# Performance work log

Measured on AMD Instinct MI355X. Metric: run time of the kernel, lower is better.

## Reference

```python
import jax, jax.numpy as jnp
import numpy as np

EPS = 1e-8
N_ITERS = 3
LN_EPS = 1e-5  # torch LayerNorm default


def layer_norm(x, g, b):
    mu = jnp.mean(x, axis=-1, keepdims=True)
    var = jnp.var(x, axis=-1, keepdims=True)
    return (x - mu) / jnp.sqrt(var + LN_EPS) * g + b


def setup_inputs() -> dict:
    key = jax.random.key(0)
    ks = jax.random.split(key, 12)
    B, S, F, D_in, D_slot, D_kvq, D_hid = 64, 16, 4096, 512, 512, 512, 2048
    p = lambda i, shape: jax.random.normal(ks[i], shape, dtype=jnp.float32) * 0.02
    return dict(
        slots=jax.random.normal(ks[0], (B, S, D_slot), dtype=jnp.float32),
        features=jax.random.normal(ks[1], (B, F, D_in), dtype=jnp.float32),
        ln_feat_g=jnp.ones((D_in,), jnp.float32), ln_feat_b=jnp.zeros((D_in,), jnp.float32),
        ln_slot_g=jnp.ones((D_slot,), jnp.float32), ln_slot_b=jnp.zeros((D_slot,), jnp.float32),
        w_k=p(2, (D_kvq, D_in)), w_v=p(3, (D_kvq, D_in)), w_q=p(4, (D_kvq, D_slot)),
        gru_w_ih=p(5, (3 * D_slot, D_kvq)), gru_w_hh=p(6, (3 * D_slot, D_slot)),
        gru_b_ih=jnp.zeros((3 * D_slot,), jnp.float32), gru_b_hh=jnp.zeros((3 * D_slot,), jnp.float32),
        mlp_ln_g=jnp.ones((D_slot,), jnp.float32), mlp_ln_b=jnp.zeros((D_slot,), jnp.float32),
        mlp_w1=p(7, (D_hid, D_slot)), mlp_b1=jnp.zeros((D_hid,), jnp.float32),
        mlp_w2=p(8, (D_slot, D_hid)), mlp_b2=jnp.zeros((D_slot,), jnp.float32),
    )


def reference(slots, features, ln_feat_g, ln_feat_b, ln_slot_g, ln_slot_b,
              w_k, w_v, w_q, gru_w_ih, gru_w_hh, gru_b_ih, gru_b_hh,
              mlp_ln_g, mlp_ln_b, mlp_w1, mlp_b1, mlp_w2, mlp_b2):
    scale = w_q.shape[0] ** -0.5  # kvq_dim**-0.5

    f = layer_norm(features, ln_feat_g, ln_feat_b)  # [B,F,D_in]
    keys = f @ w_k.T    # [B,F,D_kvq]
    values = f @ w_v.T  # [B,F,D_kvq]

    def gru_cell(x, h):  # torch.nn.GRUCell semantics
        gi = x @ gru_w_ih.T + gru_b_ih
        gh = h @ gru_w_hh.T + gru_b_hh
        i_r, i_z, i_n = jnp.split(gi, 3, axis=-1)
        h_r, h_z, h_n = jnp.split(gh, 3, axis=-1)
        r = jax.nn.sigmoid(i_r + h_r)
        z = jax.nn.sigmoid(i_z + h_z)
        n = jnp.tanh(i_n + r * h_n)
        return (1.0 - z) * n + z * h

    pre_norm_attn = None
    for _ in range(N_ITERS):  # fixed small iteration count (n_iters=3)
        s_n = layer_norm(slots, ln_slot_g, ln_slot_b)  # note: GRU hidden uses normed slots, per source
        q = s_n @ w_q.T                                 # [B,S,D_kvq]
        dots = jnp.einsum('bsd,bfd->bsf', q, keys) * scale
        pre_norm_attn = jax.nn.softmax(dots, axis=1)    # softmax over SLOT dim
        attn = pre_norm_attn + EPS
        attn = attn / jnp.sum(attn, axis=-1, keepdims=True)
        updates = jnp.einsum('bsf,bfd->bsd', attn, values)
        slots = gru_cell(updates, s_n)
        # residual MLP with initial LayerNorm
        h = layer_norm(slots, mlp_ln_g, mlp_ln_b)
        h = jax.nn.relu(h @ mlp_w1.T + mlp_b1) @ mlp_w2.T + mlp_b2
        slots = slots + h
    return slots, pre_norm_attn
```

## Files before the change

kernel.cpp:

```cpp
#include <hip/hip_runtime.h>


typedef __bf16 bf16x8 __attribute__((ext_vector_type(8)));
typedef float  f32x4  __attribute__((ext_vector_type(4)));

#define DEV static __device__ __forceinline__

DEV float bf2f_lo(unsigned int u) { union { unsigned int i; float f; } v; v.i = u << 16; return v.f; }
DEV unsigned short f2bf(float f) {
  union { float f; unsigned int i; } v; v.f = f;
  return (unsigned short)((v.i + 0x7FFFu + ((v.i >> 16) & 1u)) >> 16);
}

template<int OUTF>
__global__ __launch_bounds__(256) void ln512_kernel(
    const float* __restrict__ X, const float* __restrict__ g,
    const float* __restrict__ b, unsigned short* __restrict__ Yb,
    float* __restrict__ Yf, int R) {
  int wave = (blockIdx.x << 2) | (threadIdx.x >> 6);
  int lane = threadIdx.x & 63;
  if (wave >= R) return;
  const float4* xp = reinterpret_cast<const float4*>(X + (size_t)wave * 512);
  float4 x0 = xp[lane * 2], x1 = xp[lane * 2 + 1];
  float xv[8] = {x0.x, x0.y, x0.z, x0.w, x1.x, x1.y, x1.z, x1.w};
  float s = 0.f, q = 0.f;
#pragma unroll
  for (int j = 0; j < 8; ++j) { s += xv[j]; q += xv[j] * xv[j]; }
#pragma unroll
  for (int off = 32; off; off >>= 1) { s += __shfl_xor(s, off); q += __shfl_xor(q, off); }
  float mu = s * (1.0f / 512.0f);
  float var = q * (1.0f / 512.0f) - mu * mu;
  float rstd = rsqrtf(var + 1e-5f);
  const float4* gp = reinterpret_cast<const float4*>(g);
  const float4* bp = reinterpret_cast<const float4*>(b);
  float4 g0 = gp[lane * 2], g1 = gp[lane * 2 + 1];
  float4 b0 = bp[lane * 2], b1 = bp[lane * 2 + 1];
  float gv[8] = {g0.x, g0.y, g0.z, g0.w, g1.x, g1.y, g1.z, g1.w};
  float bv[8] = {b0.x, b0.y, b0.z, b0.w, b1.x, b1.y, b1.z, b1.w};
  float y[8];
  unsigned short u[8];
#pragma unroll
  for (int j = 0; j < 8; ++j) { y[j] = (xv[j] - mu) * rstd * gv[j] + bv[j]; u[j] = f2bf(y[j]); }
  uint4 o = make_uint4(
      (unsigned)u[0] | ((unsigned)u[1] << 16), (unsigned)u[2] | ((unsigned)u[3] << 16),
      (unsigned)u[4] | ((unsigned)u[5] << 16), (unsigned)u[6] | ((unsigned)u[7] << 16));
  reinterpret_cast<uint4*>(Yb + (size_t)wave * 512)[lane] = o;
  if (OUTF) {
    float4* yf = reinterpret_cast<float4*>(Yf + (size_t)wave * 512);
    yf[lane * 2]     = make_float4(y[0], y[1], y[2], y[3]);
    yf[lane * 2 + 1] = make_float4(y[4], y[5], y[6], y[7]);
  }
}

__global__ __launch_bounds__(256) void prep_weights_kernel(
    const float* __restrict__ w_ih, const float* __restrict__ w_hh,
    const float* __restrict__ w1, const float* __restrict__ w2,
    const float* __restrict__ w_k, const float* __restrict__ w_q,
    const float* __restrict__ w_v,
    unsigned short* __restrict__ Wih, unsigned short* __restrict__ Whh,
    unsigned short* __restrict__ W1, unsigned short* __restrict__ W2,
    unsigned short* __restrict__ WkT, unsigned short* __restrict__ WqT,
    unsigned short* __restrict__ WvT) {
  int blk = blockIdx.x, tid = threadIdx.x;
  if (blk < 3584) {
    const float* src; unsigned short* dst; int base;
    if (blk < 768)       { src = w_ih; dst = Wih; base = blk; }
    else if (blk < 1536) { src = w_hh; dst = Whh; base = blk - 768; }
    else if (blk < 2560) { src = w1;   dst = W1;  base = blk - 1536; }
    else                 { src = w2;   dst = W2;  base = blk - 2560; }
    int i = base * 256 + tid;
    float4 v = reinterpret_cast<const float4*>(src)[i];
    unsigned int lo = (unsigned)f2bf(v.x) | ((unsigned)f2bf(v.y) << 16);
    unsigned int hi = (unsigned)f2bf(v.z) | ((unsigned)f2bf(v.w) << 16);
    reinterpret_cast<uint2*>(dst)[i] = make_uint2(lo, hi);
  } else {
    int rgn = (blk - 3584) >> 10, base = (blk - 3584) & 1023;
    const float* src = rgn == 0 ? w_k : rgn == 1 ? w_q : w_v;
    unsigned short* dst = rgn == 0 ? WkT : rgn == 1 ? WqT : WvT;
    int t2 = base * 256 + tid;
    int i = t2 >> 9, j = t2 & 511;
    dst[t2] = f2bf(src[j * 512 + i]);
  }
}

template<int MODE>
__global__ __launch_bounds__(256) void gemm_nt(
    const unsigned short* __restrict__ A, const unsigned short* __restrict__ Bm,
    const float* __restrict__ bias, unsigned short* __restrict__ Cb,
    int M, int N, int K) {
  int lane = threadIdx.x & 63;
  int w = threadIdx.x >> 6;
  int m0 = blockIdx.y << 5;
  int n0 = (blockIdx.x << 7) + (w << 5);
  int lo = lane & 15, hi = lane >> 4;
  const unsigned short* Ap = A + (size_t)(m0 + lo) * K + (hi << 3);
  const unsigned short* Bp = Bm + (size_t)(n0 + lo) * K + (hi << 3);
  f32x4 acc[2][2];
#pragma unroll
  for (int i = 0; i < 2; ++i)
#pragma unroll
    for (int j = 0; j < 2; ++j) acc[i][j] = f32x4{0.f, 0.f, 0.f, 0.f};
#pragma unroll 2
  for (int kk = 0; kk < K; kk += 32) {
    bf16x8 a0 = *reinterpret_cast<const bf16x8*>(Ap + kk);
    bf16x8 a1 = *reinterpret_cast<const bf16x8*>(Ap + (size_t)16 * K + kk);
    bf16x8 b0 = *reinterpret_cast<const bf16x8*>(Bp + kk);
    bf16x8 b1 = *reinterpret_cast<const bf16x8*>(Bp + (size_t)16 * K + kk);
    acc[0][0] = __builtin_amdgcn_mfma_f32_16x16x32_bf16(a0, b0, acc[0][0], 0, 0, 0);
    acc[0][1] = __builtin_amdgcn_mfma_f32_16x16x32_bf16(a0, b1, acc[0][1], 0, 0, 0);
    acc[1][0] = __builtin_amdgcn_mfma_f32_16x16x32_bf16(a1, b0, acc[1][0], 0, 0, 0);
    acc[1][1] = __builtin_amdgcn_mfma_f32_16x16x32_bf16(a1, b1, acc[1][1], 0, 0, 0);
  }
#pragma unroll
  for (int i = 0; i < 2; ++i)
#pragma unroll
    for (int j = 0; j < 2; ++j) {
      int col = n0 + (j << 4) + lo;
      float bvv = (MODE == 3) ? bias[col] : 0.f;
#pragma unroll
      for (int r = 0; r < 4; ++r) {
        int row = m0 + (i << 4) + (hi << 2) + r;
        float v = acc[i][j][r];
        if (MODE == 0) Cb[(size_t)row * N + col] = f2bf(v);
        else           Cb[(size_t)row * N + col] = f2bf(fmaxf(v + bvv, 0.f));
      }
    }
}

template<int MODE>
__global__ __launch_bounds__(256) void gemm_nt64(
    const unsigned short* __restrict__ A, const unsigned short* __restrict__ Bm,
    const float* __restrict__ bias, const float* __restrict__ res,
    float* __restrict__ Cf, unsigned short* __restrict__ Cb,
    int M, int N, int K) {
  int lane = threadIdx.x & 63;
  int w = threadIdx.x >> 6;
  int m0 = (blockIdx.y << 5) + ((w >> 1) << 4);
  int n0 = (blockIdx.x << 6) + ((w & 1) << 5);
  int lo = lane & 15, hi = lane >> 4;
  const unsigned short* Ap = A + (size_t)(m0 + lo) * K + (hi << 3);
  const unsigned short* Bp = Bm + (size_t)(n0 + lo) * K + (hi << 3);
  f32x4 acc[2];
  acc[0] = f32x4{0.f, 0.f, 0.f, 0.f};
  acc[1] = f32x4{0.f, 0.f, 0.f, 0.f};
#pragma unroll 2
  for (int kk = 0; kk < K; kk += 32) {
    bf16x8 a0 = *reinterpret_cast<const bf16x8*>(Ap + kk);
    bf16x8 b0 = *reinterpret_cast<const bf16x8*>(Bp + kk);
    bf16x8 b1 = *reinterpret_cast<const bf16x8*>(Bp + (size_t)16 * K + kk);
    acc[0] = __builtin_amdgcn_mfma_f32_16x16x32_bf16(a0, b0, acc[0], 0, 0, 0);
    acc[1] = __builtin_amdgcn_mfma_f32_16x16x32_bf16(a0, b1, acc[1], 0, 0, 0);
  }
#pragma unroll
  for (int j = 0; j < 2; ++j) {
    int col = n0 + (j << 4) + lo;
    float bvv = (MODE == 4) ? bias[col] : 0.f;
#pragma unroll
    for (int r = 0; r < 4; ++r) {
      int row = m0 + (hi << 2) + r;
      float v = acc[j][r];
      if (MODE == 0) Cb[(size_t)row * N + col] = f2bf(v);
      else Cf[(size_t)row * N + col] = v + bvv + res[(size_t)row * N + col];
    }
  }
}

__global__ __launch_bounds__(128) void fused_attn_kernel(
    const unsigned short* __restrict__ Qp,
    const unsigned short* __restrict__ Fn,
    float* __restrict__ Upart,
    float* __restrict__ fsumP,
    float* __restrict__ attn_out) {
  __shared__ unsigned short tile[32 * 514];
  __shared__ unsigned short attn_lds[16 * 34];
  int b = blockIdx.y, g = blockIdx.x;
  int t = threadIdx.x;
  int w = t >> 6, lane = t & 63;
  int lo = lane & 15, hi = lane >> 4;
  unsigned int* tile32 = reinterpret_cast<unsigned int*>(tile);

  const unsigned short* qa = Qp + ((size_t)b * 16 + lo) * 512 + (hi << 3);
  const unsigned short* gstage = Fn + ((size_t)b * 4096 + g * 256) * 512;

  f32x4 uacc[16];
#pragma unroll
  for (int s = 0; s < 16; ++s) uacc[s] = f32x4{0.f, 0.f, 0.f, 0.f};
  float fs[4] = {0.f, 0.f, 0.f, 0.f};

  const float scale = 0.04419417382415922f;

  {
    uint4 nx[16];
#pragma unroll
    for (int k = 0; k < 16; ++k)
      nx[k] = *reinterpret_cast<const uint4*>(gstage + (size_t)t * 8 + k * 1024);
#pragma unroll
    for (int k = 0; k < 16; ++k) {
      unsigned int* p32 = tile32 + (k * 2 + w) * 257 + lane * 4;
      p32[0] = nx[k].x; p32[1] = nx[k].y; p32[2] = nx[k].z; p32[3] = nx[k].w;
    }
  }
  __syncthreads();

  for (int c = 0; c < 8; ++c) {
    uint4 nx[16];
    if (c < 7) {
      const unsigned short* src = gstage + (size_t)(c + 1) * 16384;
#pragma unroll
      for (int k = 0; k < 16; ++k)
        nx[k] = *reinterpret_cast<const uint4*>(src + (size_t)t * 8 + k * 1024);
    }
    f32x4 dacc = {0.f, 0.f, 0.f, 0.f};
#pragma unroll
    for (int ks = 0; ks < 16; ++ks) {
      const unsigned int* bp32 = tile32 + (w * 16 + lo) * 257 + ks * 16 + (hi << 2);
      union { unsigned int u[4]; bf16x8 v; } bf;
      bf.u[0] = bp32[0]; bf.u[1] = bp32[1]; bf.u[2] = bp32[2]; bf.u[3] = bp32[3];
      bf16x8 a = *reinterpret_cast<const bf16x8*>(qa + ks * 32);
      dacc = __builtin_amdgcn_mfma_f32_16x16x32_bf16(a, bf.v, dacc, 0, 0, 0);
    }
    float d4[4], mx = -3.4e38f;
#pragma unroll
    for (int r = 0; r < 4; ++r) { d4[r] = dacc[r] * scale; mx = fmaxf(mx, d4[r]); }
    mx = fmaxf(mx, __shfl_xor(mx, 16));
    mx = fmaxf(mx, __shfl_xor(mx, 32));
    float e4[4], ss = 0.f;
#pragma unroll
    for (int r = 0; r < 4; ++r) { e4[r] = __expf(d4[r] - mx); ss += e4[r]; }
    ss += __shfl_xor(ss, 16);
    ss += __shfl_xor(ss, 32);
    float inv = 1.f / ss;
    float cs[4];
#pragma unroll
    for (int r = 0; r < 4; ++r) {
      float p = e4[r] * inv;
      if (attn_out)
        attn_out[((size_t)b * 16 + (hi << 2) + r) * 4096 + g * 256 + c * 32 + (w << 4) + lo] = p;
      unsigned short uu = f2bf(p + 1e-8f);
      attn_lds[((hi << 2) + r) * 34 + (w << 4) + lo] = uu;
      cs[r] = bf2f_lo(uu);
    }
#pragma unroll
    for (int m = 1; m < 16; m <<= 1) {
#pragma unroll
      for (int r = 0; r < 4; ++r) cs[r] += __shfl_xor(cs[r], m);
    }
#pragma unroll
    for (int r = 0; r < 4; ++r) fs[r] += cs[r];
    __syncthreads();
    {
      const unsigned int* ap32 = reinterpret_cast<const unsigned int*>(attn_lds) + lo * 17 + (hi << 2);
      union { unsigned int u[4]; bf16x8 v; } paf;
      paf.u[0] = ap32[0]; paf.u[1] = ap32[1]; paf.u[2] = ap32[2]; paf.u[3] = ap32[3];
#pragma unroll
      for (int sub = 0; sub < 16; ++sub) {
        int dcol = (w << 8) + (sub << 4) + lo;
        union { unsigned short u[8]; bf16x8 v; } pbf;
#pragma unroll
        for (int j = 0; j < 8; ++j)
          pbf.u[j] = tile[((hi << 3) + j) * 514 + dcol];
        uacc[sub] = __builtin_amdgcn_mfma_f32_16x16x32_bf16(paf.v, pbf.v, uacc[sub], 0, 0, 0);
      }
    }
    __syncthreads();
    if (c < 7) {
#pragma unroll
      for (int k = 0; k < 16; ++k) {
        unsigned int* p32 = tile32 + (k * 2 + w) * 257 + lane * 4;
        p32[0] = nx[k].x; p32[1] = nx[k].y; p32[2] = nx[k].z; p32[3] = nx[k].w;
      }
      __syncthreads();
    }
  }
#pragma unroll
  for (int sub = 0; sub < 16; ++sub) {
#pragma unroll
    for (int r = 0; r < 4; ++r)
      Upart[((size_t)(b * 16 + g) * 16 + (hi << 2) + r) * 512 + (w << 8) + (sub << 4) + lo] = uacc[sub][r];
  }
  if (lo == 0) {
#pragma unroll
    for (int r = 0; r < 4; ++r)
      fsumP[((size_t)(b * 16 + g) * 2 + w) * 16 + (hi << 2) + r] = fs[r];
  }
}

__global__ void invf_kernel(const float* __restrict__ fsumP, float* __restrict__ invf) {
  int t = blockIdx.x * 256 + threadIdx.x;
  if (t >= 1024) return;
  int b = t >> 4, s = t & 15;
  const float* p = fsumP + (size_t)b * 512 + s;
  float acc = 0.f;
#pragma unroll
  for (int i = 0; i < 32; ++i) acc += p[i * 16];
  invf[t] = 1.f / acc;
}

__global__ void upd_fin_kernel(const float* __restrict__ Upart,
                               const float* __restrict__ invf,
                               unsigned short* __restrict__ outb) {
  int t = blockIdx.x * 256 + threadIdx.x;
  int b = t >> 13, rem = t & 8191;
  const float* p = Upart + (size_t)b * 131072 + rem;
  float acc = 0.f;
#pragma unroll
  for (int g = 0; g < 16; ++g) acc += p[(size_t)g * 8192];
  outb[t] = f2bf(acc * invf[t >> 9]);
}

__global__ __launch_bounds__(256) void gru_gemm_kernel(
    const unsigned short* __restrict__ Au,
    const unsigned short* __restrict__ As,
    const unsigned short* __restrict__ Wc2,
    const unsigned short* __restrict__ Whh,
    const float* __restrict__ b_ih, const float* __restrict__ b_hh,
    const float* __restrict__ snf,
    float* __restrict__ hout) {
  int lane = threadIdx.x & 63, w = threadIdx.x >> 6;
  int lo = lane & 15, hi = lane >> 4;
  int m0 = blockIdx.y << 4;
  int cw = (blockIdx.x << 7) + (w << 5);
  const unsigned short* aup = Au + (size_t)(m0 + lo) * 512 + (hi << 3);
  const unsigned short* asp = As + (size_t)(m0 + lo) * 512 + (hi << 3);
  const unsigned short* bc[2][3];
  const unsigned short* bh[2][3];
#pragma unroll
  for (int jt = 0; jt < 2; ++jt)
#pragma unroll
    for (int gt = 0; gt < 3; ++gt) {
      size_t rowoff = (size_t)(cw + jt * 16 + gt * 512 + lo) * 512 + (hi << 3);
      bc[jt][gt] = Wc2 + rowoff;
      bh[jt][gt] = Whh + rowoff;
    }
  f32x4 gi[2][3], gh[2][3];
#pragma unroll
  for (int jt = 0; jt < 2; ++jt)
#pragma unroll
    for (int gt = 0; gt < 3; ++gt) {
      gi[jt][gt] = f32x4{0.f, 0.f, 0.f, 0.f};
      gh[jt][gt] = f32x4{0.f, 0.f, 0.f, 0.f};
    }
  for (int kk = 0; kk < 512; kk += 32) {
    bf16x8 au = *reinterpret_cast<const bf16x8*>(aup + kk);
    bf16x8 as_ = *reinterpret_cast<const bf16x8*>(asp + kk);
#pragma unroll
    for (int jt = 0; jt < 2; ++jt)
#pragma unroll
      for (int gt = 0; gt < 3; ++gt) {
        bf16x8 wc = *reinterpret_cast<const bf16x8*>(bc[jt][gt] + kk);
        bf16x8 wh = *reinterpret_cast<const bf16x8*>(bh[jt][gt] + kk);
        gi[jt][gt] = __builtin_amdgcn_mfma_f32_16x16x32_bf16(au, wc, gi[jt][gt], 0, 0, 0);
        gh[jt][gt] = __builtin_amdgcn_mfma_f32_16x16x32_bf16(as_, wh, gh[jt][gt], 0, 0, 0);
      }
  }
#pragma unroll
  for (int jt = 0; jt < 2; ++jt) {
    int col = cw + (jt << 4) + lo;
    float bir = b_ih[col], biz = b_ih[col + 512], bin = b_ih[col + 1024];
    float bhr = b_hh[col], bhz = b_hh[col + 512], bhn = b_hh[col + 1024];
#pragma unroll
    for (int r = 0; r < 4; ++r) {
      int row = m0 + (hi << 2) + r;
      float rr = (gi[jt][0][r] + bir) + (gh[jt][0][r] + bhr);
      float zz = (gi[jt][1][r] + biz) + (gh[jt][1][r] + bhz);
      float rg = 1.f / (1.f + __expf(-rr));
      float zg = 1.f / (1.f + __expf(-zz));
      float a = (gi[jt][2][r] + bin) + rg * (gh[jt][2][r] + bhn);
      float ee = __expf(-2.f * fabsf(a));
      float nt = (1.f - ee) / (1.f + ee);
      float n = copysignf(nt, a);
      float hp = snf[(size_t)row * 512 + col];
      hout[(size_t)row * 512 + col] = (1.f - zg) * n + zg * hp;
    }
  }
}

extern "C" void kernel_launch(void* const* d_in, const int* in_sizes, int n_in,
                              void* d_out, int out_size, void* d_ws, size_t ws_size,
                              hipStream_t stream) {
  const float* slots_in  = (const float*)d_in[0];
  const float* features  = (const float*)d_in[1];
  const float* ln_feat_g = (const float*)d_in[2];
  const float* ln_feat_b = (const float*)d_in[3];
  const float* ln_slot_g = (const float*)d_in[4];
  const float* ln_slot_b = (const float*)d_in[5];
  const float* w_k  = (const float*)d_in[6];
  const float* w_v  = (const float*)d_in[7];
  const float* w_q  = (const float*)d_in[8];
  const float* w_ih = (const float*)d_in[9];
  const float* w_hh = (const float*)d_in[10];
  const float* b_ih = (const float*)d_in[11];
  const float* b_hh = (const float*)d_in[12];
  const float* mlp_ln_g = (const float*)d_in[13];
  const float* mlp_ln_b = (const float*)d_in[14];
  const float* w1 = (const float*)d_in[15];
  const float* b1 = (const float*)d_in[16];
  const float* w2 = (const float*)d_in[17];
  const float* b2 = (const float*)d_in[18];

  char* ws = (char*)d_ws;
  size_t off = 0;
  auto alloc = [&](size_t bytes) {
    char* p = ws + off;
    off += (bytes + 255) & ~(size_t)255;
    return p;
  };
  unsigned short* f_norm  = (unsigned short*)alloc((size_t)64 * 4096 * 512 * 2);
  unsigned short* qp_bf   = (unsigned short*)alloc(1024 * 512 * 2);
  float*          s_n_f   = (float*)alloc(1024 * 512 * 4);
  unsigned short* s_n_bf  = (unsigned short*)alloc(1024 * 512 * 2);
  float*          fsumP   = (float*)alloc(64 * 32 * 16 * 4);
  float*          invf    = (float*)alloc(1024 * 4);
  float*          Upart   = (float*)alloc((size_t)64 * 16 * 16 * 512 * 4);
  unsigned short* updp_bf = (unsigned short*)alloc(1024 * 512 * 2);
  float*          slots_c = (float*)alloc(1024 * 512 * 4);
  unsigned short* hln_bf  = (unsigned short*)alloc(1024 * 512 * 2);
  unsigned short* hm_bf   = (unsigned short*)alloc((size_t)1024 * 2048 * 2);
  unsigned short* Wqk_bf  = (unsigned short*)alloc(512 * 512 * 2);
  unsigned short* Wih_bf  = (unsigned short*)alloc(1536 * 512 * 2);
  unsigned short* Whh_bf  = (unsigned short*)alloc(1536 * 512 * 2);
  unsigned short* WkT_bf  = (unsigned short*)alloc(512 * 512 * 2);
  unsigned short* WqT_bf  = (unsigned short*)alloc(512 * 512 * 2);
  unsigned short* WvT_bf  = (unsigned short*)alloc(512 * 512 * 2);
  unsigned short* Wc2_bf  = (unsigned short*)alloc(1536 * 512 * 2);
  unsigned short* W1_bf   = (unsigned short*)alloc((size_t)2048 * 512 * 2);
  unsigned short* W2_bf   = (unsigned short*)alloc((size_t)512 * 2048 * 2);

  float* out_slots = (float*)d_out;
  float* out_attn  = out_slots + 1024 * 512;

  prep_weights_kernel<<<dim3(6656), dim3(256), 0, stream>>>(
      w_ih, w_hh, w1, w2, w_k, w_q, w_v,
      Wih_bf, Whh_bf, W1_bf, W2_bf, WkT_bf, WqT_bf, WvT_bf);
  gemm_nt<0><<<dim3(4, 16), dim3(256), 0, stream>>>(
      WkT_bf, WqT_bf, nullptr, Wqk_bf, 512, 512, 512);
  gemm_nt<0><<<dim3(4, 48), dim3(256), 0, stream>>>(
      Wih_bf, WvT_bf, nullptr, Wc2_bf, 1536, 512, 512);
  ln512_kernel<0><<<dim3(65536), dim3(256), 0, stream>>>(
      features, ln_feat_g, ln_feat_b, f_norm, nullptr, 262144);

  for (int it = 0; it < 3; ++it) {
    const float* slots_src = (it == 0) ? slots_in : slots_c;
    ln512_kernel<1><<<dim3(256), dim3(256), 0, stream>>>(
        slots_src, ln_slot_g, ln_slot_b, s_n_bf, s_n_f, 1024);
    gemm_nt64<0><<<dim3(8, 32), dim3(256), 0, stream>>>(
        s_n_bf, Wqk_bf, nullptr, nullptr, nullptr, qp_bf, 1024, 512, 512);
    fused_attn_kernel<<<dim3(16, 64), dim3(128), 0, stream>>>(
        qp_bf, f_norm, Upart, fsumP, (it == 2) ? out_attn : nullptr);
    invf_kernel<<<dim3(4), dim3(256), 0, stream>>>(fsumP, invf);
    upd_fin_kernel<<<dim3(2048), dim3(256), 0, stream>>>(Upart, invf, updp_bf);
    gru_gemm_kernel<<<dim3(4, 64), dim3(256), 0, stream>>>(
        updp_bf, s_n_bf, Wc2_bf, Whh_bf, b_ih, b_hh, s_n_f, slots_c);
    ln512_kernel<0><<<dim3(256), dim3(256), 0, stream>>>(
        slots_c, mlp_ln_g, mlp_ln_b, hln_bf, nullptr, 1024);
    gemm_nt<3><<<dim3(16, 32), dim3(256), 0, stream>>>(
        hln_bf, W1_bf, b1, hm_bf, 1024, 2048, 512);
    float* slot_dst = (it == 2) ? out_slots : slots_c;
    gemm_nt64<4><<<dim3(8, 32), dim3(256), 0, stream>>>(
        hm_bf, W2_bf, b2, slots_c, slot_dst, nullptr, 1024, 512, 2048);
  }
  (void)in_sizes; (void)n_in; (void)out_size; (void)ws_size;
}
```

Baseline: 697.5 us.

## Fuse feature LayerNorm into first attention pass and fuse slot LN with query GEMM

The first iteration's attention kernel now reads fp32 features, applies LayerNorm on the fly, feeds the normalized bf16 tile to the attention math and writes it to the f_norm buffer for later iterations. This removes the separate full-size feature LayerNorm pass and one re-read of f_norm. Slot LayerNorm and the query projection are merged into a single per-batch kernel, and the inverse-sum kernel is folded into the update finalizer. The attention block grows to 256 threads, with only two waves doing the score/softmax work, which may leave the other waves idle during that phase.

After: 817.3 us. 17.2% more time.

```diff
diff --git a/kernel.cpp b/kernel.cpp
--- a/kernel.cpp
+++ b/kernel.cpp
@@ -12,11 +12,9 @@
   return (unsigned short)((v.i + 0x7FFFu + ((v.i >> 16) & 1u)) >> 16);
 }
 
-template<int OUTF>
 __global__ __launch_bounds__(256) void ln512_kernel(
     const float* __restrict__ X, const float* __restrict__ g,
-    const float* __restrict__ b, unsigned short* __restrict__ Yb,
-    float* __restrict__ Yf, int R) {
+    const float* __restrict__ b, unsigned short* __restrict__ Yb, int R) {
   int wave = (blockIdx.x << 2) | (threadIdx.x >> 6);
   int lane = threadIdx.x & 63;
   if (wave >= R) return;
@@ -37,19 +35,13 @@
   float4 b0 = bp[lane * 2], b1 = bp[lane * 2 + 1];
   float gv[8] = {g0.x, g0.y, g0.z, g0.w, g1.x, g1.y, g1.z, g1.w};
   float bv[8] = {b0.x, b0.y, b0.z, b0.w, b1.x, b1.y, b1.z, b1.w};
-  float y[8];
   unsigned short u[8];
 #pragma unroll
-  for (int j = 0; j < 8; ++j) { y[j] = (xv[j] - mu) * rstd * gv[j] + bv[j]; u[j] = f2bf(y[j]); }
+  for (int j = 0; j < 8; ++j) u[j] = f2bf((xv[j] - mu) * rstd * gv[j] + bv[j]);
   uint4 o = make_uint4(
       (unsigned)u[0] | ((unsigned)u[1] << 16), (unsigned)u[2] | ((unsigned)u[3] << 16),
       (unsigned)u[4] | ((unsigned)u[5] << 16), (unsigned)u[6] | ((unsigned)u[7] << 16));
   reinterpret_cast<uint4*>(Yb + (size_t)wave * 512)[lane] = o;
-  if (OUTF) {
-    float4* yf = reinterpret_cast<float4*>(Yf + (size_t)wave * 512);
-    yf[lane * 2]     = make_float4(y[0], y[1], y[2], y[3]);
-    yf[lane * 2 + 1] = make_float4(y[4], y[5], y[6], y[7]);
-  }
 }
 
 __global__ __launch_bounds__(256) void prep_weights_kernel(
@@ -127,12 +119,10 @@
     }
 }
 
-template<int MODE>
-__global__ __launch_bounds__(256) void gemm_nt64(
+__global__ __launch_bounds__(256) void gemm_nt64_res(
     const unsigned short* __restrict__ A, const unsigned short* __restrict__ Bm,
     const float* __restrict__ bias, const float* __restrict__ res,
-    float* __restrict__ Cf, unsigned short* __restrict__ Cb,
-    int M, int N, int K) {
+    float* __restrict__ Cf, int M, int N, int K) {
   int lane = threadIdx.x & 63;
   int w = threadIdx.x >> 6;
   int m0 = (blockIdx.y << 5) + ((w >> 1) << 4);
@@ -154,107 +144,228 @@
 #pragma unroll
   for (int j = 0; j < 2; ++j) {
     int col = n0 + (j << 4) + lo;
-    float bvv = (MODE == 4) ? bias[col] : 0.f;
+    float bvv = bias[col];
 #pragma unroll
     for (int r = 0; r < 4; ++r) {
       int row = m0 + (hi << 2) + r;
-      float v = acc[j][r];
-      if (MODE == 0) Cb[(size_t)row * N + col] = f2bf(v);
-      else Cf[(size_t)row * N + col] = v + bvv + res[(size_t)row * N + col];
-    }
-  }
-}
-
-__global__ __launch_bounds__(128) void fused_attn_kernel(
+      Cf[(size_t)row * N + col] = acc[j][r] + bvv + res[(size_t)row * N + col];
+    }
+  }
+}
+
+__global__ __launch_bounds__(256) void lnqp_kernel(
+    const float* __restrict__ slots, const float* __restrict__ g,
+    const float* __restrict__ bta, const unsigned short* __restrict__ Wqk,
+    float* __restrict__ snf, unsigned short* __restrict__ snb,
+    unsigned short* __restrict__ qp) {
+  __shared__ unsigned short sn_lds[16 * 546];
+  unsigned int* sn32 = reinterpret_cast<unsigned int*>(sn_lds);
+  int b = blockIdx.x, t = threadIdx.x;
+  int w = t >> 6, lane = t & 63;
+  const float4* gp = reinterpret_cast<const float4*>(g) + lane * 2;
+  const float4* bp = reinterpret_cast<const float4*>(bta) + lane * 2;
+  float4 g0 = gp[0], g1 = gp[1], b0 = bp[0], b1 = bp[1];
+  float gv[8] = {g0.x, g0.y, g0.z, g0.w, g1.x, g1.y, g1.z, g1.w};
+  float bv[8] = {b0.x, b0.y, b0.z, b0.w, b1.x, b1.y, b1.z, b1.w};
+#pragma unroll
+  for (int p = 0; p < 4; ++p) {
+    int r = (p << 2) | w;
+    const float4* xp = reinterpret_cast<const float4*>(slots + ((size_t)b * 16 + r) * 512) + lane * 2;
+    float4 x0 = xp[0], x1 = xp[1];
+    float xv[8] = {x0.x, x0.y, x0.z, x0.w, x1.x, x1.y, x1.z, x1.w};
+    float s = 0.f, q = 0.f;
+#pragma unroll
+    for (int j = 0; j < 8; ++j) { s += xv[j]; q += xv[j] * xv[j]; }
+#pragma unroll
+    for (int off = 32; off; off >>= 1) { s += __shfl_xor(s, off); q += __shfl_xor(q, off); }
+    float mu = s * (1.0f / 512.0f);
+    float var = q * (1.0f / 512.0f) - mu * mu;
+    float rstd = rsqrtf(var + 1e-5f);
+    float y[8];
+    unsigned short u[8];
+#pragma unroll
+    for (int j = 0; j < 8; ++j) { y[j] = (xv[j] - mu) * rstd * gv[j] + bv[j]; u[j] = f2bf(y[j]); }
+    float4* yf = reinterpret_cast<float4*>(snf + ((size_t)b * 16 + r) * 512) + lane * 2;
+    yf[0] = make_float4(y[0], y[1], y[2], y[3]);
+    yf[1] = make_float4(y[4], y[5], y[6], y[7]);
+    unsigned int pk[4];
+#pragma unroll
+    for (int j = 0; j < 4; ++j) pk[j] = (unsigned)u[2 * j] | ((unsigned)u[2 * j + 1] << 16);
+    reinterpret_cast<uint4*>(snb + ((size_t)b * 16 + r) * 512)[lane] =
+        make_uint4(pk[0], pk[1], pk[2], pk[3]);
+    unsigned int* dst = sn32 + r * 273 + lane * 4;
+    dst[0] = pk[0]; dst[1] = pk[1]; dst[2] = pk[2]; dst[3] = pk[3];
+  }
+  __syncthreads();
+  int lo = lane & 15, hi = lane >> 4;
+  int n0 = w << 7;
+  f32x4 acc[8];
+#pragma unroll
+  for (int sub = 0; sub < 8; ++sub) acc[sub] = f32x4{0.f, 0.f, 0.f, 0.f};
+  for (int kk = 0; kk < 16; ++kk) {
+    const unsigned int* ap32 = sn32 + lo * 273 + kk * 16 + (hi << 2);
+    union { unsigned int u[4]; bf16x8 v; } af;
+    af.u[0] = ap32[0]; af.u[1] = ap32[1]; af.u[2] = ap32[2]; af.u[3] = ap32[3];
+#pragma unroll
+    for (int sub = 0; sub < 8; ++sub) {
+      const bf16x8 bw = *reinterpret_cast<const bf16x8*>(
+          Wqk + (size_t)(n0 + sub * 16 + lo) * 512 + kk * 32 + (hi << 3));
+      acc[sub] = __builtin_amdgcn_mfma_f32_16x16x32_bf16(af.v, bw, acc[sub], 0, 0, 0);
+    }
+  }
+#pragma unroll
+  for (int sub = 0; sub < 8; ++sub)
+#pragma unroll
+    for (int r = 0; r < 4; ++r)
+      qp[((size_t)b * 16 + (hi << 2) + r) * 512 + n0 + sub * 16 + lo] = f2bf(acc[sub][r]);
+}
+
+template<int LNF>
+__global__ __launch_bounds__(256) void fused_attn_kernel(
     const unsigned short* __restrict__ Qp,
     const unsigned short* __restrict__ Fn,
+    const float* __restrict__ Xf,
+    const float* __restrict__ lng, const float* __restrict__ lnb,
+    unsigned short* __restrict__ FnOut,
     float* __restrict__ Upart,
     float* __restrict__ fsumP,
     float* __restrict__ attn_out) {
   __shared__ unsigned short tile[32 * 514];
   __shared__ unsigned short attn_lds[16 * 34];
-  int b = blockIdx.y, g = blockIdx.x;
+  int b = blockIdx.y, gg = blockIdx.x;
   int t = threadIdx.x;
   int w = t >> 6, lane = t & 63;
   int lo = lane & 15, hi = lane >> 4;
+  int l6 = t & 63;
   unsigned int* tile32 = reinterpret_cast<unsigned int*>(tile);
 
   const unsigned short* qa = Qp + ((size_t)b * 16 + lo) * 512 + (hi << 3);
-  const unsigned short* gstage = Fn + ((size_t)b * 4096 + g * 256) * 512;
-
-  f32x4 uacc[16];
-#pragma unroll
-  for (int s = 0; s < 16; ++s) uacc[s] = f32x4{0.f, 0.f, 0.f, 0.f};
+  const unsigned short* gstage = (LNF == 0) ? Fn + ((size_t)b * 4096 + gg * 256) * 512 : nullptr;
+  const float* xstage = (LNF == 1) ? Xf + ((size_t)b * 4096 + gg * 256) * 512 : nullptr;
+
+  float gv[8], bvv[8];
+  if (LNF == 1) {
+    const float4* gp = reinterpret_cast<const float4*>(lng) + l6 * 2;
+    const float4* bp = reinterpret_cast<const float4*>(lnb) + l6 * 2;
+    float4 a0 = gp[0], a1 = gp[1], c0 = bp[0], c1 = bp[1];
+    gv[0] = a0.x; gv[1] = a0.y; gv[2] = a0.z; gv[3] = a0.w;
+    gv[4] = a1.x; gv[5] = a1.y; gv[6] = a1.z; gv[7] = a1.w;
+    bvv[0] = c0.x; bvv[1] = c0.y; bvv[2] = c0.z; bvv[3] = c0.w;
+    bvv[4] = c1.x; bvv[5] = c1.y; bvv[6] = c1.z; bvv[7] = c1.w;
+  }
+
+  f32x4 uacc[8];
+#pragma unroll
+  for (int s = 0; s < 8; ++s) uacc[s] = f32x4{0.f, 0.f, 0.f, 0.f};
   float fs[4] = {0.f, 0.f, 0.f, 0.f};
-
   const float scale = 0.04419417382415922f;
 
-  {
-    uint4 nx[16];
-#pragma unroll
-    for (int k = 0; k < 16; ++k)
-      nx[k] = *reinterpret_cast<const uint4*>(gstage + (size_t)t * 8 + k * 1024);
-#pragma unroll
-    for (int k = 0; k < 16; ++k) {
-      unsigned int* p32 = tile32 + (k * 2 + w) * 257 + lane * 4;
-      p32[0] = nx[k].x; p32[1] = nx[k].y; p32[2] = nx[k].z; p32[3] = nx[k].w;
+  uint4 nxb[8];
+  float4 nxf[16];
+
+  if (LNF == 0) {
+#pragma unroll
+    for (int k = 0; k < 8; ++k)
+      nxb[k] = *reinterpret_cast<const uint4*>(gstage + k * 2048 + t * 8);
+  } else {
+#pragma unroll
+    for (int k = 0; k < 8; ++k) {
+      const float4* src = reinterpret_cast<const float4*>(xstage + k * 2048 + t * 8);
+      nxf[2 * k] = src[0]; nxf[2 * k + 1] = src[1];
+    }
+  }
+#pragma unroll
+  for (int k = 0; k < 8; ++k) {
+    int rk = (k << 2) | w;
+    unsigned int* dst = tile32 + rk * 257 + l6 * 4;
+    if (LNF == 0) {
+      dst[0] = nxb[k].x; dst[1] = nxb[k].y; dst[2] = nxb[k].z; dst[3] = nxb[k].w;
+    } else {
+      float4 v0 = nxf[2 * k], v1 = nxf[2 * k + 1];
+      float xv[8] = {v0.x, v0.y, v0.z, v0.w, v1.x, v1.y, v1.z, v1.w};
+      float s = 0.f, q = 0.f;
+#pragma unroll
+      for (int j = 0; j < 8; ++j) { s += xv[j]; q += xv[j] * xv[j]; }
+#pragma unroll
+      for (int off = 32; off; off >>= 1) { s += __shfl_xor(s, off); q += __shfl_xor(q, off); }
+      float mu = s * (1.0f / 512.0f);
+      float rstd = rsqrtf(q * (1.0f / 512.0f) - mu * mu + 1e-5f);
+      unsigned short u[8];
+#pragma unroll
+      for (int j = 0; j < 8; ++j) u[j] = f2bf((xv[j] - mu) * rstd * gv[j] + bvv[j]);
+      unsigned int pk[4];
+#pragma unroll
+      for (int j = 0; j < 4; ++j) pk[j] = (unsigned)u[2 * j] | ((unsigned)u[2 * j + 1] << 16);
+      dst[0] = pk[0]; dst[1] = pk[1]; dst[2] = pk[2]; dst[3] = pk[3];
+      *reinterpret_cast<uint4*>(FnOut + ((size_t)b * 4096 + gg * 256 + rk) * 512 + (l6 << 3)) =
+          make_uint4(pk[0], pk[1], pk[2], pk[3]);
     }
   }
   __syncthreads();
 
   for (int c = 0; c < 8; ++c) {
-    uint4 nx[16];
     if (c < 7) {
-      const unsigned short* src = gstage + (size_t)(c + 1) * 16384;
-#pragma unroll
-      for (int k = 0; k < 16; ++k)
-        nx[k] = *reinterpret_cast<const uint4*>(src + (size_t)t * 8 + k * 1024);
-    }
-    f32x4 dacc = {0.f, 0.f, 0.f, 0.f};
-#pragma unroll
-    for (int ks = 0; ks < 16; ++ks) {
-      const unsigned int* bp32 = tile32 + (w * 16 + lo) * 257 + ks * 16 + (hi << 2);
-      union { unsigned int u[4]; bf16x8 v; } bf;
-      bf.u[0] = bp32[0]; bf.u[1] = bp32[1]; bf.u[2] = bp32[2]; bf.u[3] = bp32[3];
-      bf16x8 a = *reinterpret_cast<const bf16x8*>(qa + ks * 32);
-      dacc = __builtin_amdgcn_mfma_f32_16x16x32_bf16(a, bf.v, dacc, 0, 0, 0);
-    }
-    float d4[4], mx = -3.4e38f;
-#pragma unroll
-    for (int r = 0; r < 4; ++r) { d4[r] = dacc[r] * scale; mx = fmaxf(mx, d4[r]); }
-    mx = fmaxf(mx, __shfl_xor(mx, 16));
-    mx = fmaxf(mx, __shfl_xor(mx, 32));
-    float e4[4], ss = 0.f;
-#pragma unroll
-    for (int r = 0; r < 4; ++r) { e4[r] = __expf(d4[r] - mx); ss += e4[r]; }
-    ss += __shfl_xor(ss, 16);
-    ss += __shfl_xor(ss, 32);
-    float inv = 1.f / ss;
-    float cs[4];
-#pragma unroll
-    for (int r = 0; r < 4; ++r) {
-      float p = e4[r] * inv;
-      if (attn_out)
-        attn_out[((size_t)b * 16 + (hi << 2) + r) * 4096 + g * 256 + c * 32 + (w << 4) + lo] = p;
-      unsigned short uu = f2bf(p + 1e-8f);
-      attn_lds[((hi << 2) + r) * 34 + (w << 4) + lo] = uu;
-      cs[r] = bf2f_lo(uu);
-    }
-#pragma unroll
-    for (int m = 1; m < 16; m <<= 1) {
-#pragma unroll
-      for (int r = 0; r < 4; ++r) cs[r] += __shfl_xor(cs[r], m);
-    }
-#pragma unroll
-    for (int r = 0; r < 4; ++r) fs[r] += cs[r];
+      if (LNF == 0) {
+        const unsigned short* src = gstage + (size_t)(c + 1) * 16384;
+#pragma unroll
+        for (int k = 0; k < 8; ++k)
+          nxb[k] = *reinterpret_cast<const uint4*>(src + k * 2048 + t * 8);
+      } else {
+        const float* src = xstage + (size_t)(c + 1) * 16384;
+#pragma unroll
+        for (int k = 0; k < 8; ++k) {
+          const float4* sp = reinterpret_cast<const float4*>(src + k * 2048 + t * 8);
+          nxf[2 * k] = sp[0]; nxf[2 * k + 1] = sp[1];
+        }
+      }
+    }
+    if (w < 2) {
+      f32x4 dacc = {0.f, 0.f, 0.f, 0.f};
+#pragma unroll
+      for (int ks = 0; ks < 16; ++ks) {
+        const unsigned int* bp32 = tile32 + (w * 16 + lo) * 257 + ks * 16 + (hi << 2);
+        union { unsigned int u[4]; bf16x8 v; } bf;
+        bf.u[0] = bp32[0]; bf.u[1] = bp32[1]; bf.u[2] = bp32[2]; bf.u[3] = bp32[3];
+        bf16x8 a = *reinterpret_cast<const bf16x8*>(qa + ks * 32);
+        dacc = __builtin_amdgcn_mfma_f32_16x16x32_bf16(a, bf.v, dacc, 0, 0, 0);
+      }
+      float d4[4], mx = -3.4e38f;
+#pragma unroll
+      for (int r = 0; r < 4; ++r) { d4[r] = dacc[r] * scale; mx = fmaxf(mx, d4[r]); }
+      mx = fmaxf(mx, __shfl_xor(mx, 16));
+      mx = fmaxf(mx, __shfl_xor(mx, 32));
+      float e4[4], ss = 0.f;
+#pragma unroll
+      for (int r = 0; r < 4; ++r) { e4[r] = __expf(d4[r] - mx); ss += e4[r]; }
+      ss += __shfl_xor(ss, 16);
+      ss += __shfl_xor(ss, 32);
+      float inv = 1.f / ss;
+      float cs[4];
+#pragma unroll
+      for (int r = 0; r < 4; ++r) {
+        float p = e4[r] * inv;
+        if (attn_out)
+          attn_out[((size_t)b * 16 + (hi << 2) + r) * 4096 + gg * 256 + c * 32 + (w << 4) + lo] = p;
+        unsigned short uu = f2bf(p + 1e-8f);
+        attn_lds[((hi << 2) + r) * 34 + (w << 4) + lo] = uu;
+        cs[r] = bf2f_lo(uu);
+      }
+#pragma unroll
+      for (int m = 1; m < 16; m <<= 1) {
+#pragma unroll
+        for (int r = 0; r < 4; ++r) cs[r] += __shfl_xor(cs[r], m);
+      }
+#pragma unroll
+      for (int r = 0; r < 4; ++r) fs[r] += cs[r];
+    }
     __syncthreads();
     {
       const unsigned int* ap32 = reinterpret_cast<const unsigned int*>(attn_lds) + lo * 17 + (hi << 2);
       union { unsigned int u[4]; bf16x8 v; } paf;
       paf.u[0] = ap32[0]; paf.u[1] = ap32[1]; paf.u[2] = ap32[2]; paf.u[3] = ap32[3];
 #pragma unroll
-      for (int sub = 0; sub < 16; ++sub) {
-        int dcol = (w << 8) + (sub << 4) + lo;
+      for (int sub = 0; sub < 8; ++sub) {
+        int dcol = (w << 7) + (sub << 4) + lo;
         union { unsigned short u[8]; bf16x8 v; } pbf;
 #pragma unroll
         for (int j = 0; j < 8; ++j)
@@ -265,57 +376,73 @@
     __syncthreads();
     if (c < 7) {
 #pragma unroll
-      for (int k = 0; k < 16; ++k) {
-        unsigned int* p32 = tile32 + (k * 2 + w) * 257 + lane * 4;
-        p32[0] = nx[k].x; p32[1] = nx[k].y; p32[2] = nx[k].z; p32[3] = nx[k].w;
+      for (int k = 0; k < 8; ++k) {
+        int rk = (k << 2) | w;
+        unsigned int* dst = tile32 + rk * 257 + l6 * 4;
+        if (LNF == 0) {
+          dst[0] = nxb[k].x; dst[1] = nxb[k].y; dst[2] = nxb[k].z; dst[3] = nxb[k].w;
+        } else {
+          float4 v0 = nxf[2 * k], v1 = nxf[2 * k + 1];
+          float xv[8] = {v0.x, v0.y, v0.z, v0.w, v1.x, v1.y, v1.z, v1.w};
+          float s = 0.f, q = 0.f;
+#pragma unroll
+          for (int j = 0; j < 8; ++j) { s += xv[j]; q += xv[j] * xv[j]; }
+#pragma unroll
+          for (int off = 32; off; off >>= 1) { s += __shfl_xor(s, off); q += __shfl_xor(q, off); }
+          float mu = s * (1.0f / 512.0f);
+          float rstd = rsqrtf(q * (1.0f / 512.0f) - mu * mu + 1e-5f);
+          unsigned short u[8];
+#pragma unroll
+          for (int j = 0; j < 8; ++j) u[j] = f2bf((xv[j] - mu) * rstd * gv[j] + bvv[j]);
+          unsigned int pk[4];
+#pragma unroll
+          for (int j = 0; j < 4; ++j) pk[j] = (unsigned)u[2 * j] | ((unsigned)u[2 * j + 1] << 16);
+          dst[0] = pk[0]; dst[1] = pk[1]; dst[2] = pk[2]; dst[3] = pk[3];
+          *reinterpret_cast<uint4*>(
+              FnOut + ((size_t)b * 4096 + gg * 256 + (c + 1) * 32 + rk) * 512 + (l6 << 3)) =
+              make_uint4(pk[0], pk[1], pk[2], pk[3]);
+        }
       }
       __syncthreads();
     }
   }
 #pragma unroll
-  for (int sub = 0; sub < 16; ++sub) {
+  for (int sub = 0; sub < 8; ++sub) {
 #pragma unroll
     for (int r = 0; r < 4; ++r)
-      Upart[((size_t)(b * 16 + g) * 16 + (hi << 2) + r) * 512 + (w << 8) + (sub << 4) + lo] = uacc[sub][r];
-  }
-  if (lo == 0) {
+      Upart[((size_t)(b * 16 + gg) * 16 + (hi << 2) + r) * 512 + (w << 7) + (sub << 4) + lo] =
+          uacc[sub][r];
+  }
+  if (w < 2 && lo == 0) {
 #pragma unroll
     for (int r = 0; r < 4; ++r)
-      fsumP[((size_t)(b * 16 + g) * 2 + w) * 16 + (hi << 2) + r] = fs[r];
-  }
-}
-
-__global__ void invf_kernel(const float* __restrict__ fsumP, float* __restrict__ invf) {
-  int t = blockIdx.x * 256 + threadIdx.x;
-  if (t >= 1024) return;
-  int b = t >> 4, s = t & 15;
-  const float* p = fsumP + (size_t)b * 512 + s;
+      fsumP[((size_t)(b * 16 + gg) * 2 + w) * 16 + (hi << 2) + r] = fs[r];
+  }
+}
+
+__global__ __launch_bounds__(256) void upd_fin_kernel(
+    const float* __restrict__ Upart, const float* __restrict__ fsumP,
+    unsigned short* __restrict__ outb) {
+  int blk = blockIdx.x;
+  int b = blk >> 5;
+  int s = (blk >> 1) & 15;
+  int d = ((blk & 1) << 8) + threadIdx.x;
+  float fsum = 0.f;
+#pragma unroll
+  for (int i = 0; i < 32; ++i) fsum += fsumP[(size_t)b * 512 + i * 16 + s];
+  float inv = 1.f / fsum;
+  const float* p = Upart + (size_t)b * 131072 + s * 512 + d;
   float acc = 0.f;
 #pragma unroll
-  for (int i = 0; i < 32; ++i) acc += p[i * 16];
-  invf[t] = 1.f / acc;
-}
-
-__global__ void upd_fin_kernel(const float* __restrict__ Upart,
-                               const float* __restrict__ invf,
-                               unsigned short* __restrict__ outb) {
-  int t = blockIdx.x * 256 + threadIdx.x;
-  int b = t >> 13, rem = t & 8191;
-  const float* p = Upart + (size_t)b * 131072 + rem;
-  float acc = 0.f;
-#pragma unroll
   for (int g = 0; g < 16; ++g) acc += p[(size_t)g * 8192];
-  outb[t] = f2bf(acc * invf[t >> 9]);
+  outb[((size_t)b * 16 + s) * 512 + d] = f2bf(acc * inv);
 }
 
 __global__ __launch_bounds__(256) void gru_gemm_kernel(
-    const unsigned short* __restrict__ Au,
-    const unsigned short* __restrict__ As,
-    const unsigned short* __restrict__ Wc2,
-    const unsigned short* __restrict__ Whh,
+    const unsigned short* __restrict__ Au, const unsigned short* __restrict__ As,
+    const unsigned short* __restrict__ Wc2, const unsigned short* __restrict__ Whh,
     const float* __restrict__ b_ih, const float* __restrict__ b_hh,
-    const float* __restrict__ snf,
-    float* __restrict__ hout) {
+    const float* __restrict__ snf, float* __restrict__ hout) {
   int lane = threadIdx.x & 63, w = threadIdx.x >> 6;
   int lo = lane & 15, hi = lane >> 4;
   int m0 = blockIdx.y << 4;
@@ -410,7 +537,6 @@
   float*          s_n_f   = (float*)alloc(1024 * 512 * 4);
   unsigned short* s_n_bf  = (unsigned short*)alloc(1024 * 512 * 2);
   float*          fsumP   = (float*)alloc(64 * 32 * 16 * 4);
-  float*          invf    = (float*)alloc(1024 * 4);
   float*          Upart   = (float*)alloc((size_t)64 * 16 * 16 * 512 * 4);
   unsigned short* updp_bf = (unsigned short*)alloc(1024 * 512 * 2);
   float*          slots_c = (float*)alloc(1024 * 512 * 4);
@@ -436,28 +562,30 @@
       WkT_bf, WqT_bf, nullptr, Wqk_bf, 512, 512, 512);
   gemm_nt<0><<<dim3(4, 48), dim3(256), 0, stream>>>(
       Wih_bf, WvT_bf, nullptr, Wc2_bf, 1536, 512, 512);
-  ln512_kernel<0><<<dim3(65536), dim3(256), 0, stream>>>(
-      features, ln_feat_g, ln_feat_b, f_norm, nullptr, 262144);
 
   for (int it = 0; it < 3; ++it) {
     const float* slots_src = (it == 0) ? slots_in : slots_c;
-    ln512_kernel<1><<<dim3(256), dim3(256), 0, stream>>>(
-        slots_src, ln_slot_g, ln_slot_b, s_n_bf, s_n_f, 1024);
-    gemm_nt64<0><<<dim3(8, 32), dim3(256), 0, stream>>>(
-        s_n_bf, Wqk_bf, nullptr, nullptr, nullptr, qp_bf, 1024, 512, 512);
-    fused_attn_kernel<<<dim3(16, 64), dim3(128), 0, stream>>>(
-        qp_bf, f_norm, Upart, fsumP, (it == 2) ? out_attn : nullptr);
-    invf_kernel<<<dim3(4), dim3(256), 0, stream>>>(fsumP, invf);
-    upd_fin_kernel<<<dim3(2048), dim3(256), 0, stream>>>(Upart, invf, updp_bf);
+    lnqp_kernel<<<dim3(64), dim3(256), 0, stream>>>(
+        slots_src, ln_slot_g, ln_slot_b, Wqk_bf, s_n_f, s_n_bf, qp_bf);
+    if (it == 0) {
+      fused_attn_kernel<1><<<dim3(16, 64), dim3(256), 0, stream>>>(
+          qp_bf, nullptr, features, ln_feat_g, ln_feat_b, f_norm,
+          Upart, fsumP, nullptr);
+    } else {
+      fused_attn_kernel<0><<<dim3(16, 64), dim3(256), 0, stream>>>(
+          qp_bf, f_norm, nullptr, nullptr, nullptr, nullptr,
+          Upart, fsumP, (it == 2) ? out_attn : nullptr);
+    }
+    upd_fin_kernel<<<dim3(2048), dim3(256), 0, stream>>>(Upart, fsumP, updp_bf);
     gru_gemm_kernel<<<dim3(4, 64), dim3(256), 0, stream>>>(
         updp_bf, s_n_bf, Wc2_bf, Whh_bf, b_ih, b_hh, s_n_f, slots_c);
-    ln512_kernel<0><<<dim3(256), dim3(256), 0, stream>>>(
-        slots_c, mlp_ln_g, mlp_ln_b, hln_bf, nullptr, 1024);
+    ln512_kernel<<<dim3(256), dim3(256), 0, stream>>>(
+        slots_c, mlp_ln_g, mlp_ln_b, hln_bf, 1024);
     gemm_nt<3><<<dim3(16, 32), dim3(256), 0, stream>>>(
         hln_bf, W1_bf, b1, hm_bf, 1024, 2048, 512);
     float* slot_dst = (it == 2) ? out_slots : slots_c;
-    gemm_nt64<4><<<dim3(8, 32), dim3(256), 0, stream>>>(
-        hm_bf, W2_bf, b2, slots_c, slot_dst, nullptr, 1024, 512, 2048);
+    gemm_nt64_res<<<dim3(8, 32), dim3(256), 0, stream>>>(
+        hm_bf, W2_bf, b2, slots_c, slot_dst, 1024, 512, 2048);
   }
   (void)in_sizes; (void)n_in; (void)out_size; (void)ws_size;
 }
```

## Fuse MLP GEMMs through LDS and merge normalization-sum into update finalize

Applied to the files above, without the earlier changes.

Replaces the two-kernel MLP (W1 GEMM with ReLU writing a bf16 hidden buffer, then W2 GEMM with bias and residual) by one kernel per 16-row tile that keeps the 16x2048 hidden activations in swizzled shared memory. It also folds the per-slot attention-sum reciprocal into the update-finalize kernel, removing a launch and the invf buffer. This removes the hidden-activation global round trip and two launches per iteration. In exchange the MLP now runs on only 64 blocks, each re-reading both full weight matrices, so parallelism is much lower.

Result: slower. 1.023 ms (+46.6%).

```diff
diff --git a/kernel.cpp b/kernel.cpp
--- a/kernel.cpp
+++ b/kernel.cpp
@@ -116,23 +116,17 @@
 #pragma unroll
     for (int j = 0; j < 2; ++j) {
       int col = n0 + (j << 4) + lo;
-      float bvv = (MODE == 3) ? bias[col] : 0.f;
 #pragma unroll
       for (int r = 0; r < 4; ++r) {
         int row = m0 + (i << 4) + (hi << 2) + r;
-        float v = acc[i][j][r];
-        if (MODE == 0) Cb[(size_t)row * N + col] = f2bf(v);
-        else           Cb[(size_t)row * N + col] = f2bf(fmaxf(v + bvv, 0.f));
+        Cb[(size_t)row * N + col] = f2bf(acc[i][j][r]);
       }
     }
 }
 
-template<int MODE>
-__global__ __launch_bounds__(256) void gemm_nt64(
+__global__ __launch_bounds__(256) void gemm_nt64_bf(
     const unsigned short* __restrict__ A, const unsigned short* __restrict__ Bm,
-    const float* __restrict__ bias, const float* __restrict__ res,
-    float* __restrict__ Cf, unsigned short* __restrict__ Cb,
-    int M, int N, int K) {
+    unsigned short* __restrict__ Cb, int M, int N, int K) {
   int lane = threadIdx.x & 63;
   int w = threadIdx.x >> 6;
   int m0 = (blockIdx.y << 5) + ((w >> 1) << 4);
@@ -154,13 +148,10 @@
 #pragma unroll
   for (int j = 0; j < 2; ++j) {
     int col = n0 + (j << 4) + lo;
-    float bvv = (MODE == 4) ? bias[col] : 0.f;
 #pragma unroll
     for (int r = 0; r < 4; ++r) {
       int row = m0 + (hi << 2) + r;
-      float v = acc[j][r];
-      if (MODE == 0) Cb[(size_t)row * N + col] = f2bf(v);
-      else Cf[(size_t)row * N + col] = v + bvv + res[(size_t)row * N + col];
+      Cb[(size_t)row * N + col] = f2bf(acc[j][r]);
     }
   }
 }
@@ -285,37 +276,29 @@
   }
 }
 
-__global__ void invf_kernel(const float* __restrict__ fsumP, float* __restrict__ invf) {
-  int t = blockIdx.x * 256 + threadIdx.x;
-  if (t >= 1024) return;
-  int b = t >> 4, s = t & 15;
-  const float* p = fsumP + (size_t)b * 512 + s;
+__global__ __launch_bounds__(256) void upd_fin_kernel(
+    const float* __restrict__ Upart, const float* __restrict__ fsumP,
+    unsigned short* __restrict__ outb) {
+  int blk = blockIdx.x;
+  int b = blk >> 5;
+  int s = (blk >> 1) & 15;
+  int d = ((blk & 1) << 8) + threadIdx.x;
+  float fsum = 0.f;
+#pragma unroll
+  for (int i = 0; i < 32; ++i) fsum += fsumP[(size_t)b * 512 + i * 16 + s];
+  float inv = 1.f / fsum;
+  const float* p = Upart + (size_t)b * 131072 + s * 512 + d;
   float acc = 0.f;
 #pragma unroll
-  for (int i = 0; i < 32; ++i) acc += p[i * 16];
-  invf[t] = 1.f / acc;
-}
-
-__global__ void upd_fin_kernel(const float* __restrict__ Upart,
-                               const float* __restrict__ invf,
-                               unsigned short* __restrict__ outb) {
-  int t = blockIdx.x * 256 + threadIdx.x;
-  int b = t >> 13, rem = t & 8191;
-  const float* p = Upart + (size_t)b * 131072 + rem;
-  float acc = 0.f;
-#pragma unroll
   for (int g = 0; g < 16; ++g) acc += p[(size_t)g * 8192];
-  outb[t] = f2bf(acc * invf[t >> 9]);
+  outb[((size_t)b * 16 + s) * 512 + d] = f2bf(acc * inv);
 }
 
 __global__ __launch_bounds__(256) void gru_gemm_kernel(
-    const unsigned short* __restrict__ Au,
-    const unsigned short* __restrict__ As,
-    const unsigned short* __restrict__ Wc2,
-    const unsigned short* __restrict__ Whh,
+    const unsigned short* __restrict__ Au, const unsigned short* __restrict__ As,
+    const unsigned short* __restrict__ Wc2, const unsigned short* __restrict__ Whh,
     const float* __restrict__ b_ih, const float* __restrict__ b_hh,
-    const float* __restrict__ snf,
-    float* __restrict__ hout) {
+    const float* __restrict__ snf, float* __restrict__ hout) {
   int lane = threadIdx.x & 63, w = threadIdx.x >> 6;
   int lo = lane & 15, hi = lane >> 4;
   int m0 = blockIdx.y << 4;
@@ -371,6 +354,74 @@
       float n = copysignf(nt, a);
       float hp = snf[(size_t)row * 512 + col];
       hout[(size_t)row * 512 + col] = (1.f - zg) * n + zg * hp;
+    }
+  }
+}
+
+__global__ __launch_bounds__(256) void mlp12_kernel(
+    const unsigned short* __restrict__ A,
+    const unsigned short* __restrict__ W1,
+    const unsigned short* __restrict__ W2,
+    const float* __restrict__ b1, const float* __restrict__ b2,
+    const float* __restrict__ res,
+    float* __restrict__ out) {
+  __shared__ unsigned short hm[16 * 2048];
+  int m0 = blockIdx.x << 4;
+  int t = threadIdx.x, w = t >> 6, lane = t & 63;
+  int lo = lane & 15, hi = lane >> 4;
+  const unsigned short* Ap = A + (size_t)(m0 + lo) * 512 + (hi << 3);
+#pragma unroll
+  for (int half = 0; half < 2; ++half) {
+    int n0 = (w << 9) + (half << 8);
+    f32x4 acc[16];
+#pragma unroll
+    for (int sub = 0; sub < 16; ++sub) acc[sub] = f32x4{0.f, 0.f, 0.f, 0.f};
+    for (int kk = 0; kk < 512; kk += 32) {
+      bf16x8 a = *reinterpret_cast<const bf16x8*>(Ap + kk);
+#pragma unroll
+      for (int sub = 0; sub < 16; ++sub) {
+        bf16x8 bw = *reinterpret_cast<const bf16x8*>(
+            W1 + (size_t)(n0 + sub * 16 + lo) * 512 + kk + (hi << 3));
+        acc[sub] = __builtin_amdgcn_mfma_f32_16x16x32_bf16(a, bw, acc[sub], 0, 0, 0);
+      }
+    }
+#pragma unroll
+    for (int sub = 0; sub < 16; ++sub) {
+      int col = n0 + (sub << 4) + lo;
+      float bvv = b1[col];
+#pragma unroll
+      for (int r = 0; r < 4; ++r) {
+        int row = (hi << 2) + r;
+        hm[(row << 11) + (col ^ ((row & 7) << 3))] = f2bf(fmaxf(acc[sub][r] + bvv, 0.f));
+      }
+    }
+  }
+  __syncthreads();
+  int n0b = w << 7;
+  f32x4 acc2[8];
+#pragma unroll
+  for (int sub = 0; sub < 8; ++sub) acc2[sub] = f32x4{0.f, 0.f, 0.f, 0.f};
+  for (int kk = 0; kk < 2048; kk += 32) {
+    int kofs = kk + (hi << 3);
+    const uint4* ap = reinterpret_cast<const uint4*>(
+        &hm[(lo << 11) + (kofs ^ ((lo & 7) << 3))]);
+    union { uint4 q; bf16x8 v; } af;
+    af.q = *ap;
+#pragma unroll
+    for (int sub = 0; sub < 8; ++sub) {
+      bf16x8 bw = *reinterpret_cast<const bf16x8*>(
+          W2 + (size_t)(n0b + sub * 16 + lo) * 2048 + kofs);
+      acc2[sub] = __builtin_amdgcn_mfma_f32_16x16x32_bf16(af.v, bw, acc2[sub], 0, 0, 0);
+    }
+  }
+#pragma unroll
+  for (int sub = 0; sub < 8; ++sub) {
+    int col = n0b + (sub << 4) + lo;
+    float bvv = b2[col];
+#pragma unroll
+    for (int r = 0; r < 4; ++r) {
+      int row = m0 + (hi << 2) + r;
+      out[(size_t)row * 512 + col] = acc2[sub][r] + bvv + res[(size_t)row * 512 + col];
     }
   }
 }
@@ -410,12 +461,10 @@
   float*          s_n_f   = (float*)alloc(1024 * 512 * 4);
   unsigned short* s_n_bf  = (unsigned short*)alloc(1024 * 512 * 2);
   float*          fsumP   = (float*)alloc(64 * 32 * 16 * 4);
-  float*          invf    = (float*)alloc(1024 * 4);
   float*          Upart   = (float*)alloc((size_t)64 * 16 * 16 * 512 * 4);
   unsigned short* updp_bf = (unsigned short*)alloc(1024 * 512 * 2);
   float*          slots_c = (float*)alloc(1024 * 512 * 4);
   unsigned short* hln_bf  = (unsigned short*)alloc(1024 * 512 * 2);
-  unsigned short* hm_bf   = (unsigned short*)alloc((size_t)1024 * 2048 * 2);
   unsigned short* Wqk_bf  = (unsigned short*)alloc(512 * 512 * 2);
   unsigned short* Wih_bf  = (unsigned short*)alloc(1536 * 512 * 2);
   unsigned short* Whh_bf  = (unsigned short*)alloc(1536 * 512 * 2);
@@ -443,21 +492,18 @@
     const float* slots_src = (it == 0) ? slots_in : slots_c;
     ln512_kernel<1><<<dim3(256), dim3(256), 0, stream>>>(
         slots_src, ln_slot_g, ln_slot_b, s_n_bf, s_n_f, 1024);
-    gemm_nt64<0><<<dim3(8, 32), dim3(256), 0, stream>>>(
-        s_n_bf, Wqk_bf, nullptr, nullptr, nullptr, qp_bf, 1024, 512, 512);
+    gemm_nt64_bf<<<dim3(8, 32), dim3(256), 0, stream>>>(
+        s_n_bf, Wqk_bf, qp_bf, 1024, 512, 512);
     fused_attn_kernel<<<dim3(16, 64), dim3(128), 0, stream>>>(
         qp_bf, f_norm, Upart, fsumP, (it == 2) ? out_attn : nullptr);
-    invf_kernel<<<dim3(4), dim3(256), 0, stream>>>(fsumP, invf);
-    upd_fin_kernel<<<dim3(2048), dim3(256), 0, stream>>>(Upart, invf, updp_bf);
+    upd_fin_kernel<<<dim3(2048), dim3(256), 0, stream>>>(Upart, fsumP, updp_bf);
     gru_gemm_kernel<<<dim3(4, 64), dim3(256), 0, stream>>>(
         updp_bf, s_n_bf, Wc2_bf, Whh_bf, b_ih, b_hh, s_n_f, slots_c);
     ln512_kernel<0><<<dim3(256), dim3(256), 0, stream>>>(
         slots_c, mlp_ln_g, mlp_ln_b, hln_bf, nullptr, 1024);
-    gemm_nt<3><<<dim3(16, 32), dim3(256), 0, stream>>>(
-        hln_bf, W1_bf, b1, hm_bf, 1024, 2048, 512);
     float* slot_dst = (it == 2) ? out_slots : slots_c;
-    gemm_nt64<4><<<dim3(8, 32), dim3(256), 0, stream>>>(
-        hm_bf, W2_bf, b2, slots_c, slot_dst, nullptr, 1024, 512, 2048);
+    mlp12_kernel<<<dim3(64), dim3(256), 0, stream>>>(
+        hln_bf, W1_bf, W2_bf, b1, b2, slots_c, slot_dst);
   }
   (void)in_sizes; (void)n_in; (void)out_size; (void)ws_size;
 }
```
